# Kernel optimization log

Hardware: AMD Instinct MI355X
Metric: run time of the kernel (lower is better)

The kernel has to match this reference:

```python
import jax, jax.numpy as jnp
import numpy as np

B, F, K = 8192, 39, 16

def setup_inputs() -> dict:
    key = jax.random.key(0)
    inputs = jax.random.normal(key, (B, F, F, K), dtype=jnp.float32)
    return {"inputs": inputs}

def reference(inputs) -> jnp.ndarray:
    # Faithful FFM pairwise interaction:
    # sum_{i<j} sum_k inputs[:,i,j,k] * inputs[:,j,i,k]  -> [B, 1]
    f = inputs.shape[1]
    # elementwise product with field-transposed tensor, fused reduction
    prod = jnp.sum(inputs * jnp.swapaxes(inputs, 1, 2), axis=-1)  # [B, f, f]
    mask = jnp.triu(jnp.ones((f, f), dtype=prod.dtype), k=1)      # strict upper triangle (i<j)
    return jnp.sum(prod * mask, axis=(1, 2), keepdims=True)[:, :1]  # [B, 1]
```

## Files before the change

kernel.cpp:

```cpp
#include <hip/hip_runtime.h>


#define FF    39
#define KK    16
#define NPAIR (FF * (FF - 1) / 2)
#define SLICE (FF * FF * KK)
#define ITEMS (NPAIR * 4)
#define NTHR  256

__global__ __launch_bounds__(NTHR) void ffm_kernel(const float* __restrict__ in,
                                                   float* __restrict__ out,
                                                   int nbatch) {
    __shared__ int xoff[NPAIR];
    __shared__ int yoff[NPAIR];
    __shared__ float red[NTHR / 64];

    const int tid = threadIdx.x;

    for (int p = tid; p < NPAIR; p += NTHR) {
        int pp = p, i = 0;
        while (pp >= FF - 1 - i) { pp -= FF - 1 - i; ++i; }
        int j = i + 1 + pp;
        xoff[p] = (i * FF + j) * KK;
        yoff[p] = (j * FF + i) * KK;
    }
    __syncthreads();

    for (int b = blockIdx.x; b < nbatch; b += gridDim.x) {
        const float* base = in + (size_t)b * SLICE;
        float acc = 0.f;

        for (int item = tid; item < ITEMS; item += NTHR) {
            int p = item >> 2;
            int q = (item & 3) * 4;
            const float4 x = *reinterpret_cast<const float4*>(base + xoff[p] + q);
            const float4 y = *reinterpret_cast<const float4*>(base + yoff[p] + q);
            acc += x.x * y.x + x.y * y.y + x.z * y.z + x.w * y.w;
        }

        #pragma unroll
        for (int off = 32; off > 0; off >>= 1)
            acc += __shfl_down(acc, off, 64);

        const int wave = tid >> 6;
        if ((tid & 63) == 0) red[wave] = acc;
        __syncthreads();
        if (tid == 0) {
            float s = 0.f;
            #pragma unroll
            for (int w = 0; w < NTHR / 64; ++w) s += red[w];
            out[b] = s;
        }
        __syncthreads();
    }
}

extern "C" void kernel_launch(void* const* d_in, const int* in_sizes, int n_in,
                              void* d_out, int out_size, void* d_ws, size_t ws_size,
                              hipStream_t stream) {
    const float* in = (const float*)d_in[0];
    float* out = (float*)d_out;
    const int nbatch = out_size;

    dim3 grid(nbatch);
    dim3 block(NTHR);
    ffm_kernel<<<grid, block, 0, stream>>>(in, out, nbatch);
}
```

Measured before the change: 137.3 us.

## Stage upper-triangle blocks in LDS and read lower triangle in row order

The kernel now does two phases. First it copies the upper-triangle (i<j) K-vectors into shared memory, reading them in row-major order. Then it reads the lower-triangle (j,i) vectors in their own row-major order and pairs each with the matching stashed block. This is meant to make global reads more sequential than the old interleaved x/y gather, and it replaces the shared offset tables with closed-form sqrt index decoding. It adds a barrier, about 47KB of LDS per block (which limits occupancy), and extra integer math per item.

Measured after the change: 210.9 us. 1.54x slower.

```diff
diff --git a/kernel.cpp b/kernel.cpp
--- a/kernel.cpp
+++ b/kernel.cpp
@@ -3,55 +3,59 @@
 
 #define FF    39
 #define KK    16
-#define NPAIR (FF * (FF - 1) / 2)
+#define NBLK  (FF * (FF - 1) / 2)
+#define ITEMS (NBLK * 4)
 #define SLICE (FF * FF * KK)
-#define ITEMS (NPAIR * 4)
 #define NTHR  256
 
 __global__ __launch_bounds__(NTHR) void ffm_kernel(const float* __restrict__ in,
                                                    float* __restrict__ out,
                                                    int nbatch) {
-    __shared__ int xoff[NPAIR];
-    __shared__ int yoff[NPAIR];
+    __shared__ float stash[NBLK * KK];
     __shared__ float red[NTHR / 64];
 
     const int tid = threadIdx.x;
+    const int b = blockIdx.x;
+    if (b >= nbatch) return;
+    const float* base = in + (size_t)b * SLICE;
 
-    for (int p = tid; p < NPAIR; p += NTHR) {
-        int pp = p, i = 0;
-        while (pp >= FF - 1 - i) { pp -= FF - 1 - i; ++i; }
-        int j = i + 1 + pp;
-        xoff[p] = (i * FF + j) * KK;
-        yoff[p] = (j * FF + i) * KK;
+    for (int m = tid; m < ITEMS; m += NTHR) {
+        const int mb = m >> 2;
+        const int q  = m & 3;
+        int i = (int)((77.0f - sqrtf((float)(5929 - 8 * mb))) * 0.5f);
+        while (i * (77 - i) / 2 > mb) --i;
+        while ((i + 1) * (76 - i) / 2 <= mb) ++i;
+        const int j = i + 1 + (mb - i * (77 - i) / 2);
+        const float4 x = *reinterpret_cast<const float4*>(base + (i * FF + j) * KK + q * 4);
+        *reinterpret_cast<float4*>(&stash[mb * KK + q * 4]) = x;
     }
     __syncthreads();
 
-    for (int b = blockIdx.x; b < nbatch; b += gridDim.x) {
-        const float* base = in + (size_t)b * SLICE;
-        float acc = 0.f;
+    float acc = 0.f;
+    for (int m = tid; m < ITEMS; m += NTHR) {
+        const int mb = m >> 2;
+        const int q  = m & 3;
+        int j = (int)((1.0f + sqrtf((float)(1 + 8 * mb))) * 0.5f);
+        while (j * (j - 1) / 2 > mb) --j;
+        while (j * (j + 1) / 2 <= mb) ++j;
+        const int i = mb - j * (j - 1) / 2;
+        const float4 x = *reinterpret_cast<const float4*>(base + (j * FF + i) * KK + q * 4);
+        const int tU = i * (77 - i) / 2 + (j - i - 1);
+        const float4 y = *reinterpret_cast<const float4*>(&stash[tU * KK + q * 4]);
+        acc += x.x * y.x + x.y * y.y + x.z * y.z + x.w * y.w;
+    }
 
-        for (int item = tid; item < ITEMS; item += NTHR) {
-            int p = item >> 2;
-            int q = (item & 3) * 4;
-            const float4 x = *reinterpret_cast<const float4*>(base + xoff[p] + q);
-            const float4 y = *reinterpret_cast<const float4*>(base + yoff[p] + q);
-            acc += x.x * y.x + x.y * y.y + x.z * y.z + x.w * y.w;
-        }
-
+    #pragma unroll
+    for (int off = 32; off > 0; off >>= 1)
+        acc += __shfl_down(acc, off, 64);
+    const int wave = tid >> 6;
+    if ((tid & 63) == 0) red[wave] = acc;
+    __syncthreads();
+    if (tid == 0) {
+        float s = 0.f;
         #pragma unroll
-        for (int off = 32; off > 0; off >>= 1)
-            acc += __shfl_down(acc, off, 64);
-
-        const int wave = tid >> 6;
-        if ((tid & 63) == 0) red[wave] = acc;
-        __syncthreads();
-        if (tid == 0) {
-            float s = 0.f;
-            #pragma unroll
-            for (int w = 0; w < NTHR / 64; ++w) s += red[w];
-            out[b] = s;
-        }
-        __syncthreads();
+        for (int w = 0; w < NTHR / 64; ++w) s += red[w];
+        out[b] = s;
     }
 }
 
@@ -62,7 +66,5 @@
     float* out = (float*)d_out;
     const int nbatch = out_size;
 
-    dim3 grid(nbatch);
-    dim3 block(NTHR);
-    ffm_kernel<<<grid, block, 0, stream>>>(in, out, nbatch);
+    ffm_kernel<<<dim3(nbatch), dim3(NTHR), 0, stream>>>(in, out, nbatch);
 }
```
